# Performance work log

Measured on AMD Instinct MI355X. Metric: run time of the kernel, lower is better.

## Reference

```python
import jax, jax.numpy as jnp
import numpy as np
import math

N_HEADS = 16
D_EFF = 64
ROPE_BASE = 500.0


def _rope(x, cos, sin):
    # x: (b, h, L, d_eff); cos/sin: (L, d_eff//2)
    x_even = x[..., 0::2]
    x_odd = x[..., 1::2]
    rot = jnp.stack([x_even * cos - x_odd * sin,
                     x_even * sin + x_odd * cos], axis=-1)
    return rot.reshape(x.shape)


def setup_inputs() -> dict:
    key = jax.random.key(0)
    ks = jax.random.split(key, 5)
    B, L, D = 1, 2048, 1024
    X = jax.random.normal(ks[0], (B, L, D), dtype=jnp.float32)
    # causal mask (1 = keep, 0 = masked), broadcastable to (B, h, L, L)
    mask = jnp.tril(jnp.ones((L, L), dtype=jnp.int32))[None, :, :]
    s = 1.0 / math.sqrt(D)
    Wq = jax.random.normal(ks[1], (D, D), dtype=jnp.float32) * s
    Wk = jax.random.normal(ks[2], (D, D), dtype=jnp.float32) * s
    Wv = jax.random.normal(ks[3], (D, D), dtype=jnp.float32) * s
    Wo = jax.random.normal(ks[4], (D, D), dtype=jnp.float32) * s
    return {"X": X, "mask": mask, "Wq": Wq, "Wk": Wk, "Wv": Wv, "Wo": Wo}


def reference(X, mask, Wq, Wk, Wv, Wo):
    b, L, d_model = X.shape
    h, d = N_HEADS, D_EFF
    d_full = h * d

    def split_heads(Y):
        return Y.reshape(b, L, h, d).transpose(0, 2, 1, 3)  # (b,h,L,d)

    Q = split_heads(X @ Wq)
    K = split_heads(X @ Wk)
    V = split_heads(X @ Wv)

    # interleaved RoPE, base 500
    inv_freq = 1.0 / (ROPE_BASE ** (jnp.arange(0, d, 2, dtype=jnp.float32) / d))
    freqs = jnp.arange(L, dtype=jnp.float32)[:, None] * inv_freq  # (L, d/2)
    cos, sin = jnp.cos(freqs), jnp.sin(freqs)
    Q = _rope(Q, cos, sin)
    K = _rope(K, cos, sin)

    S = jnp.einsum('bhqd,bhkd->bhqk', Q, K) / math.sqrt(d)
    S = jnp.where(mask[:, None, :, :] == 0, jnp.float32(-1e9), S)
    # NOTE: faithful to original torch code: softmax over the HEADS axis (dim=1)
    A = jax.nn.softmax(S, axis=1)
    Y = jnp.einsum('bhqk,bhkd->bhqd', A, V)
    Y = Y.transpose(0, 2, 1, 3).reshape(b, L, d_full)
    Y = Y @ Wo
    return Y * math.sqrt(d_model / d_full)
```

## Files before the change

### kernel.cpp

```cpp
#include <hip/hip_runtime.h>
#include <stdint.h>
#include <stddef.h>

typedef __attribute__((ext_vector_type(8))) short bf16x8;
typedef __attribute__((ext_vector_type(4))) short short4v;
typedef __attribute__((ext_vector_type(4))) float f32x4;

__device__ __forceinline__ short f2bf(float f) {
  union { float f; uint32_t u; } x; x.f = f;
  return (short)((x.u + 0x7fffu + ((x.u >> 16) & 1u)) >> 16);
}
__device__ __forceinline__ float bf2f(short s) {
  union { uint32_t u; float f; } x; x.u = ((uint32_t)(uint16_t)s) << 16;
  return x.f;
}

__device__ __forceinline__ void gload_lds16(const void* g, void* lds) {
  __builtin_amdgcn_global_load_lds(
      (const __attribute__((address_space(1))) void*)g,
      (__attribute__((address_space(3))) void*)lds, 16, 0, 0);
}

__global__ __launch_bounds__(256) void cast_b(const float* __restrict__ s,
                                              short* __restrict__ d) {
  int i4 = (blockIdx.x * 256 + threadIdx.x) * 4;
  float4 v = *(const float4*)&s[i4];
  short4v r = { f2bf(v.x), f2bf(v.y), f2bf(v.z), f2bf(v.w) };
  *(short4v*)&d[i4] = r;
}

__global__ __launch_bounds__(256) void cast_add4(const short* __restrict__ Y0,
                                                 const short* __restrict__ Y1,
                                                 const short* __restrict__ Y2,
                                                 const short* __restrict__ Y3,
                                                 const float* __restrict__ Cvs,
                                                 short* __restrict__ o) {
  int i4 = (blockIdx.x * 256 + threadIdx.x) * 4;
  short4v a = *(const short4v*)&Y0[i4];
  short4v b = *(const short4v*)&Y1[i4];
  short4v c = *(const short4v*)&Y2[i4];
  short4v d = *(const short4v*)&Y3[i4];
  short4v r;
#pragma unroll
  for (int j = 0; j < 4; j++) {
    float s = bf2f(a[j]) + bf2f(b[j]) + bf2f(c[j]) + bf2f(d[j]) +
              Cvs[(i4 + j) & 1023];
    r[j] = f2bf(s);
  }
  *(short4v*)&o[i4] = r;
}

__global__ __launch_bounds__(256) void transW(const float* __restrict__ Wq,
                                              const float* __restrict__ Wk,
                                              const float* __restrict__ Wv,
                                              const float* __restrict__ Wo,
                                              short* __restrict__ WcatT,
                                              short* __restrict__ WoT) {
  int z = blockIdx.z;
  const float* src = (z == 0) ? Wq : (z == 1) ? Wk : (z == 2) ? Wv : Wo;
  short* dst = (z == 3) ? WoT : WcatT + (size_t)z * 1024 * 1024;
  __shared__ float tl[32][33];
  int tx = threadIdx.x & 31, ty = threadIdx.x >> 5;
  int kk0 = blockIdx.x * 32;
  int nn0 = blockIdx.y * 32;
#pragma unroll
  for (int j = 0; j < 4; j++)
    tl[ty + j * 8][tx] = src[(size_t)(kk0 + ty + j * 8) * 1024 + nn0 + tx];
  __syncthreads();
#pragma unroll
  for (int j = 0; j < 4; j++)
    dst[(size_t)(nn0 + ty + j * 8) * 1024 + kk0 + tx] = f2bf(tl[tx][ty + j * 8]);
}

__global__ __launch_bounds__(256) void transpose_v(const short* __restrict__ Vb,
                                                   short* __restrict__ Vt) {
  __shared__ short tv[64][72];
  int h = blockIdx.y, k0 = blockIdx.x * 64;
  int tid = threadIdx.x;
#pragma unroll
  for (int j = 0; j < 2; j++) {
    int idx = tid + j * 256;
    int row = idx >> 3, c = idx & 7;
    bf16x8 v = *(const bf16x8*)&Vb[((size_t)h * 2048 + k0 + row) * 64 + c * 8];
#pragma unroll
    for (int t = 0; t < 8; t++) tv[row][c * 8 + t] = v[t];
  }
  __syncthreads();
#pragma unroll
  for (int j = 0; j < 2; j++) {
    int idx = tid + j * 256;
    int d = idx >> 3, c = idx & 7;
    bf16x8 v;
#pragma unroll
    for (int t = 0; t < 8; t++) v[t] = tv[c * 8 + t][d];
    *(bf16x8*)&Vt[((size_t)h * 64 + d) * 2048 + k0 + c * 8] = v;
  }
}

__global__ __launch_bounds__(256) void vsum(const short* __restrict__ Vb,
                                            float* __restrict__ Cvs) {
  __shared__ float red[16][17];
  int h = blockIdx.x >> 2, dq = blockIdx.x & 3;
  int dl = threadIdx.x & 15, ks = threadIdx.x >> 4;
  int d = dq * 16 + dl;
  float acc = 0.f;
  const short* base = &Vb[((size_t)h * 2048 + ks * 128) * 64 + d];
#pragma unroll 8
  for (int k = 0; k < 128; k++) acc += bf2f(base[(size_t)k * 64]);
  red[dl][ks] = acc;
  __syncthreads();
  if (threadIdx.x < 16) {
    float sum = 0.f;
#pragma unroll
    for (int i = 0; i < 16; i++) sum += red[threadIdx.x][i];
    Cvs[h * 64 + dq * 16 + threadIdx.x] = sum * 0.0625f;
  }
}

template <int MODE, int TM>
__global__ __launch_bounds__(256, TM == 128 ? 2 : 4)
void gemm_kernel(const short* __restrict__ A, const short* __restrict__ B,
                 int N, int K, float* __restrict__ C,
                 short* __restrict__ Qb, short* __restrict__ Kb,
                 short* __restrict__ Vb) {
  constexpr int MT = TM / 32;
  constexpr int MSUB = TM / 2;
  __shared__ __attribute__((aligned(16))) short lga[TM * 64];
  __shared__ __attribute__((aligned(16))) short lgb[128 * 64];
  const int tid = threadIdx.x;
  const int lane = tid & 63;
  const int w = tid >> 6;
  const int l15 = lane & 15;
  const int quad = lane >> 4;
  const int wm = w >> 1, wn = w & 1;
  const int m0 = blockIdx.x * TM, n0 = blockIdx.y * 128;
  const int rsub = lane >> 3;
  const int cpos = lane & 7;

  f32x4 acc[MT][4];
#pragma unroll
  for (int i = 0; i < MT; i++)
#pragma unroll
    for (int j = 0; j < 4; j++) acc[i][j] = (f32x4){0.f, 0.f, 0.f, 0.f};

  for (int kb = 0; kb < K; kb += 64) {
    __syncthreads();
#pragma unroll
    for (int j = 0; j < TM / 32; j++) {
      int ci = w * (TM / 32) + j;
      int r = ci * 8 + rsub;
      int kc = cpos ^ rsub;
      gload_lds16(A + (size_t)(m0 + r) * K + kb + kc * 8, &lga[ci * 512]);
    }
#pragma unroll
    for (int j = 0; j < 4; j++) {
      int ci = w * 4 + j;
      int r = ci * 8 + rsub;
      int kc = cpos ^ rsub;
      gload_lds16(B + (size_t)(n0 + r) * K + kb + kc * 8, &lgb[ci * 512]);
    }
    __syncthreads();
#pragma unroll
    for (int kk = 0; kk < 2; kk++) {
      bf16x8 af[MT], bfr[4];
#pragma unroll
      for (int t = 0; t < MT; t++) {
        int row = wm * MSUB + t * 16 + l15;
        int pc = (kk * 4 + quad) ^ (row & 7);
        af[t] = *(const bf16x8*)&lga[row * 64 + pc * 8];
      }
#pragma unroll
      for (int t = 0; t < 4; t++) {
        int rowb = wn * 64 + t * 16 + l15;
        int pcb = (kk * 4 + quad) ^ (rowb & 7);
        bfr[t] = *(const bf16x8*)&lgb[rowb * 64 + pcb * 8];
      }
#pragma unroll
      for (int mt = 0; mt < MT; mt++)
#pragma unroll
        for (int nt = 0; nt < 4; nt++)
          acc[mt][nt] = __builtin_amdgcn_mfma_f32_16x16x32_bf16(
              af[mt], bfr[nt], acc[mt][nt], 0, 0, 0);
    }
  }

  if (MODE == 0) {
#pragma unroll
    for (int mt = 0; mt < MT; mt++) {
      int q = m0 + wm * MSUB + mt * 16 + quad * 4;
#pragma unroll
      for (int nt = 0; nt < 4; nt++) {
        int n = n0 + wn * 64 + nt * 16 + l15;
#pragma unroll
        for (int r = 0; r < 4; r++) C[(size_t)(q + r) * N + n] = acc[mt][nt][r];
      }
    }
  } else {
#pragma unroll
    for (int mt = 0; mt < MT; mt++) {
#pragma unroll
      for (int nt = 0; nt < 4; nt++) {
        int n = n0 + wn * 64 + nt * 16 + l15;
        int mat = n >> 10;
        int h = (n >> 6) & 15;
        int d = n & 63;
#pragma unroll
        for (int r = 0; r < 4; r++) {
          int q = m0 + wm * MSUB + mt * 16 + quad * 4 + r;
          float v = acc[mt][nt][r];
          float o = __shfl_xor(v, 1, 64);
          if (mat < 2) {
            int i = d >> 1;
            float ang = (float)q * __builtin_exp2f(-(float)i * 0.2801807588956902f);
            float sn, cs;
            __sincosf(ang, &sn, &cs);
            float rv = (d & 1) ? (o * sn + v * cs) : (v * cs - o * sn);
            short* dst = (mat == 0) ? Qb : Kb;
            dst[((size_t)h * 2048 + q) * 64 + d] = f2bf(rv);
          } else {
            Vb[((size_t)h * 2048 + q) * 64 + d] = f2bf(v);
          }
        }
      }
    }
  }
}

__global__ __launch_bounds__(1024, 8)
void attn_kernel(const short* __restrict__ Qb, const short* __restrict__ Kb,
                 const short* __restrict__ Vt, short* __restrict__ Yp) {
  __shared__ short Sb[16 * 16 * 72];
  const int tid = threadIdx.x;
  const int lane = tid & 63;
  const int h = tid >> 6;
  const int l15 = lane & 15, quad = lane >> 4;
  const int bx = blockIdx.x;
  const int qt = 127 - (bx >> 2);
  const int s = bx & 3;
  const int q0 = qt * 16;
  const int G = (qt + 4) >> 2;

  bf16x8 qf[2];
#pragma unroll
  for (int c = 0; c < 2; c++)
    qf[c] = *(const bf16x8*)&Qb[((size_t)h * 2048 + q0 + l15) * 64 + c * 32 + quad * 8];

  f32x4 yacc[4];
#pragma unroll
  for (int j = 0; j < 4; j++) yacc[j] = (f32x4){0.f, 0.f, 0.f, 0.f};

  const int sq = tid >> 6;
  const int sbase = sq * 72 + lane;

  for (int g = s; g < G; g += 4) {
    const int k0 = g * 64;
#pragma unroll
    for (int st = 0; st < 4; st++) {
      const short* kb = &Kb[((size_t)h * 2048 + k0 + st * 16 + l15) * 64 + quad * 8];
      bf16x8 kf0 = *(const bf16x8*)kb;
      bf16x8 kf1 = *(const bf16x8*)(kb + 32);
      f32x4 sa = (f32x4){0.f, 0.f, 0.f, 0.f};
      sa = __builtin_amdgcn_mfma_f32_16x16x32_bf16(qf[0], kf0, sa, 0, 0, 0);
      sa = __builtin_amdgcn_mfma_f32_16x16x32_bf16(qf[1], kf1, sa, 0, 0, 0);
#pragma unroll
      for (int r = 0; r < 4; r++)
        Sb[h * 1152 + (quad * 4 + r) * 72 + st * 16 + l15] =
            f2bf(sa[r] * 0.1803368801f);
    }
    __syncthreads();
    {
      bool msk = (k0 + lane) > (q0 + sq);
      float e[16];
      float sum = 0.f;
#pragma unroll
      for (int hh = 0; hh < 16; hh++) {
        e[hh] = __builtin_exp2f(bf2f(Sb[hh * 1152 + sbase]));
        sum += e[hh];
      }
      float rs = 1.f / sum;
#pragma unroll
      for (int hh = 0; hh < 16; hh++)
        Sb[hh * 1152 + sbase] = msk ? (short)0 : f2bf(e[hh] * rs - 0.0625f);
    }
    __syncthreads();
#pragma unroll
    for (int kk = 0; kk < 2; kk++) {
      bf16x8 af = *(const bf16x8*)&Sb[(h * 16 + l15) * 72 + kk * 32 + quad * 8];
#pragma unroll
      for (int nt = 0; nt < 4; nt++) {
        bf16x8 vf = *(const bf16x8*)&Vt[((size_t)h * 64 + nt * 16 + l15) * 2048 +
                                        k0 + kk * 32 + quad * 8];
        yacc[nt] = __builtin_amdgcn_mfma_f32_16x16x32_bf16(af, vf, yacc[nt], 0, 0, 0);
      }
    }
    __syncthreads();
  }
  short* Y = Yp + (size_t)s * 2048 * 1024;
#pragma unroll
  for (int nt = 0; nt < 4; nt++) {
    int col = h * 64 + nt * 16 + l15;
#pragma unroll
    for (int r = 0; r < 4; r++)
      Y[(size_t)(q0 + quad * 4 + r) * 1024 + col] = f2bf(yacc[nt][r]);
  }
}

extern "C" void kernel_launch(void* const* d_in, const int* in_sizes, int n_in,
                              void* d_out, int out_size, void* d_ws, size_t ws_size,
                              hipStream_t stream) {
  (void)in_sizes; (void)n_in; (void)out_size; (void)ws_size;
  const float* X  = (const float*)d_in[0];
  const float* Wq = (const float*)d_in[2];
  const float* Wk = (const float*)d_in[3];
  const float* Wv = (const float*)d_in[4];
  const float* Wo = (const float*)d_in[5];
  char* ws = (char*)d_ws;
  const size_t MB = 1024 * 1024;
  short* Xbf   = (short*)(ws + 0);
  short* WcatT = (short*)(ws + 4 * MB);
  short* WoT   = (short*)(ws + 10 * MB);
  short* Qb    = (short*)(ws + 12 * MB);
  short* Kb    = (short*)(ws + 16 * MB);
  short* Vb    = (short*)(ws + 20 * MB);
  short* Vt    = (short*)(ws + 24 * MB);
  short* Yp    = (short*)(ws + 28 * MB);
  float* Cvs   = (float*)(ws + 44 * MB);
  short* Ycbf  = Xbf;
  float* out   = (float*)d_out;

  cast_b<<<dim3(2048), dim3(256), 0, stream>>>(X, Xbf);
  transW<<<dim3(32, 32, 4), dim3(256), 0, stream>>>(Wq, Wk, Wv, Wo, WcatT, WoT);
  gemm_kernel<1, 128><<<dim3(16, 24), dim3(256), 0, stream>>>(
      Xbf, WcatT, 3072, 1024, nullptr, Qb, Kb, Vb);
  transpose_v<<<dim3(32, 16), dim3(256), 0, stream>>>(Vb, Vt);
  vsum<<<dim3(64), dim3(256), 0, stream>>>(Vb, Cvs);
  attn_kernel<<<dim3(512), dim3(1024), 0, stream>>>(Qb, Kb, Vt, Yp);
  cast_add4<<<dim3(2048), dim3(256), 0, stream>>>(Yp, Yp + 2048 * 1024,
                                                  Yp + 2 * 2048 * 1024,
                                                  Yp + 3 * 2048 * 1024, Cvs, Ycbf);
  gemm_kernel<0, 64><<<dim3(32, 8), dim3(256), 0, stream>>>(
      Ycbf, WoT, 1024, 1024, out, nullptr, nullptr, nullptr);
}
```

Before: 235.6 us.

## Enlarge attention query tile to 64 and reduce key splits via float atomics

The attention kernel now processes 64 query rows per block (four 16-row tiles) against 32-key chunks, so each K and V fragment load is reused across four MFMA row tiles. The key range is split eight ways across blocks, and partial outputs are combined with float atomicAdd into a zeroed fp32 buffer instead of four bf16 partial buffers. This lets the final combine kernel read one fp32 array. The cost is an extra memset, atomic contention and nondeterministic summation order, plus more registers per thread with a lower occupancy hint.

Result: slower. 256.5 us (+8.9%).

```diff
diff --git a/kernel.cpp b/kernel.cpp
--- a/kernel.cpp
+++ b/kernel.cpp
@@ -29,24 +29,15 @@
   *(short4v*)&d[i4] = r;
 }
 
-__global__ __launch_bounds__(256) void cast_add4(const short* __restrict__ Y0,
-                                                 const short* __restrict__ Y1,
-                                                 const short* __restrict__ Y2,
-                                                 const short* __restrict__ Y3,
+__global__ __launch_bounds__(256) void cast_addY(const float* __restrict__ Y,
                                                  const float* __restrict__ Cvs,
                                                  short* __restrict__ o) {
   int i4 = (blockIdx.x * 256 + threadIdx.x) * 4;
-  short4v a = *(const short4v*)&Y0[i4];
-  short4v b = *(const short4v*)&Y1[i4];
-  short4v c = *(const short4v*)&Y2[i4];
-  short4v d = *(const short4v*)&Y3[i4];
-  short4v r;
-#pragma unroll
-  for (int j = 0; j < 4; j++) {
-    float s = bf2f(a[j]) + bf2f(b[j]) + bf2f(c[j]) + bf2f(d[j]) +
-              Cvs[(i4 + j) & 1023];
-    r[j] = f2bf(s);
-  }
+  float4 v = *(const float4*)&Y[i4];
+  short4v r = { f2bf(v.x + Cvs[i4 & 1023]),
+                f2bf(v.y + Cvs[(i4 + 1) & 1023]),
+                f2bf(v.z + Cvs[(i4 + 2) & 1023]),
+                f2bf(v.w + Cvs[(i4 + 3) & 1023]) };
   *(short4v*)&o[i4] = r;
 }
 
@@ -226,82 +217,97 @@
   }
 }
 
-__global__ __launch_bounds__(1024, 8)
+__global__ __launch_bounds__(1024, 4)
 void attn_kernel(const short* __restrict__ Qb, const short* __restrict__ Kb,
-                 const short* __restrict__ Vt, short* __restrict__ Yp) {
-  __shared__ short Sb[16 * 16 * 72];
+                 const short* __restrict__ Vt, float* __restrict__ Y) {
+  __shared__ short Sb[16 * 64 * 40];
   const int tid = threadIdx.x;
   const int lane = tid & 63;
   const int h = tid >> 6;
   const int l15 = lane & 15, quad = lane >> 4;
-  const int bx = blockIdx.x;
-  const int qt = 127 - (bx >> 2);
-  const int s = bx & 3;
-  const int q0 = qt * 16;
-  const int G = (qt + 4) >> 2;
-
-  bf16x8 qf[2];
-#pragma unroll
-  for (int c = 0; c < 2; c++)
-    qf[c] = *(const bf16x8*)&Qb[((size_t)h * 2048 + q0 + l15) * 64 + c * 32 + quad * 8];
-
-  f32x4 yacc[4];
-#pragma unroll
-  for (int j = 0; j < 4; j++) yacc[j] = (f32x4){0.f, 0.f, 0.f, 0.f};
-
-  const int sq = tid >> 6;
-  const int sbase = sq * 72 + lane;
-
-  for (int g = s; g < G; g += 4) {
-    const int k0 = g * 64;
-#pragma unroll
-    for (int st = 0; st < 4; st++) {
+  const int qt = 31 - (blockIdx.x >> 3);
+  const int s = blockIdx.x & 7;
+  const int q0 = qt * 64;
+  const int C = 2 * qt + 2;
+
+  bf16x8 qf[4][2];
+#pragma unroll
+  for (int mt = 0; mt < 4; mt++)
+#pragma unroll
+    for (int c = 0; c < 2; c++)
+      qf[mt][c] = *(const bf16x8*)&Qb[((size_t)h * 2048 + q0 + mt * 16 + l15) * 64 +
+                                      c * 32 + quad * 8];
+
+  f32x4 yacc[4][4];
+#pragma unroll
+  for (int i = 0; i < 4; i++)
+#pragma unroll
+    for (int j = 0; j < 4; j++) yacc[i][j] = (f32x4){0.f, 0.f, 0.f, 0.f};
+
+  for (int g = s; g < C; g += 8) {
+    const int k0 = g * 32;
+#pragma unroll
+    for (int st = 0; st < 2; st++) {
       const short* kb = &Kb[((size_t)h * 2048 + k0 + st * 16 + l15) * 64 + quad * 8];
       bf16x8 kf0 = *(const bf16x8*)kb;
       bf16x8 kf1 = *(const bf16x8*)(kb + 32);
-      f32x4 sa = (f32x4){0.f, 0.f, 0.f, 0.f};
-      sa = __builtin_amdgcn_mfma_f32_16x16x32_bf16(qf[0], kf0, sa, 0, 0, 0);
-      sa = __builtin_amdgcn_mfma_f32_16x16x32_bf16(qf[1], kf1, sa, 0, 0, 0);
-#pragma unroll
-      for (int r = 0; r < 4; r++)
-        Sb[h * 1152 + (quad * 4 + r) * 72 + st * 16 + l15] =
-            f2bf(sa[r] * 0.1803368801f);
-    }
-    __syncthreads();
-    {
-      bool msk = (k0 + lane) > (q0 + sq);
+#pragma unroll
+      for (int mt = 0; mt < 4; mt++) {
+        f32x4 sa = (f32x4){0.f, 0.f, 0.f, 0.f};
+        sa = __builtin_amdgcn_mfma_f32_16x16x32_bf16(qf[mt][0], kf0, sa, 0, 0, 0);
+        sa = __builtin_amdgcn_mfma_f32_16x16x32_bf16(qf[mt][1], kf1, sa, 0, 0, 0);
+#pragma unroll
+        for (int r = 0; r < 4; r++)
+          Sb[(h * 64 + mt * 16 + quad * 4 + r) * 40 + st * 16 + l15] =
+              f2bf(sa[r] * 0.1803368801f);
+      }
+    }
+    __syncthreads();
+#pragma unroll
+    for (int pp = 0; pp < 2; pp++) {
+      int p = tid + pp * 1024;
+      int q = p >> 5, kl = p & 31;
+      int base = q * 40 + kl;
       float e[16];
       float sum = 0.f;
 #pragma unroll
       for (int hh = 0; hh < 16; hh++) {
-        e[hh] = __builtin_exp2f(bf2f(Sb[hh * 1152 + sbase]));
+        e[hh] = __builtin_exp2f(bf2f(Sb[hh * 2560 + base]));
         sum += e[hh];
       }
       float rs = 1.f / sum;
+      bool msk = (k0 + kl) > (q0 + q);
 #pragma unroll
       for (int hh = 0; hh < 16; hh++)
-        Sb[hh * 1152 + sbase] = msk ? (short)0 : f2bf(e[hh] * rs - 0.0625f);
-    }
-    __syncthreads();
-#pragma unroll
-    for (int kk = 0; kk < 2; kk++) {
-      bf16x8 af = *(const bf16x8*)&Sb[(h * 16 + l15) * 72 + kk * 32 + quad * 8];
+        Sb[hh * 2560 + base] = msk ? (short)0 : f2bf(e[hh] * rs - 0.0625f);
+    }
+    __syncthreads();
+    bf16x8 vf[4];
+#pragma unroll
+    for (int nt = 0; nt < 4; nt++)
+      vf[nt] = *(const bf16x8*)&Vt[((size_t)(h * 64 + nt * 16 + l15)) * 2048 +
+                                   k0 + quad * 8];
+#pragma unroll
+    for (int mt = 0; mt < 4; mt++) {
+      bf16x8 af = *(const bf16x8*)&Sb[(h * 64 + mt * 16 + l15) * 40 + quad * 8];
+#pragma unroll
+      for (int nt = 0; nt < 4; nt++)
+        yacc[mt][nt] = __builtin_amdgcn_mfma_f32_16x16x32_bf16(af, vf[nt],
+                                                               yacc[mt][nt], 0, 0, 0);
+    }
+    __syncthreads();
+  }
+  if (s < C) {
+#pragma unroll
+    for (int mt = 0; mt < 4; mt++)
 #pragma unroll
       for (int nt = 0; nt < 4; nt++) {
-        bf16x8 vf = *(const bf16x8*)&Vt[((size_t)h * 64 + nt * 16 + l15) * 2048 +
-                                        k0 + kk * 32 + quad * 8];
-        yacc[nt] = __builtin_amdgcn_mfma_f32_16x16x32_bf16(af, vf, yacc[nt], 0, 0, 0);
-      }
-    }
-    __syncthreads();
-  }
-  short* Y = Yp + (size_t)s * 2048 * 1024;
-#pragma unroll
-  for (int nt = 0; nt < 4; nt++) {
-    int col = h * 64 + nt * 16 + l15;
-#pragma unroll
-    for (int r = 0; r < 4; r++)
-      Y[(size_t)(q0 + quad * 4 + r) * 1024 + col] = f2bf(yacc[nt][r]);
+        int col = h * 64 + nt * 16 + l15;
+#pragma unroll
+        for (int r = 0; r < 4; r++)
+          atomicAdd(&Y[(size_t)(q0 + mt * 16 + quad * 4 + r) * 1024 + col],
+                    yacc[mt][nt][r]);
+      }
   }
 }
 
@@ -323,21 +329,20 @@
   short* Kb    = (short*)(ws + 16 * MB);
   short* Vb    = (short*)(ws + 20 * MB);
   short* Vt    = (short*)(ws + 24 * MB);
-  short* Yp    = (short*)(ws + 28 * MB);
-  float* Cvs   = (float*)(ws + 44 * MB);
+  float* Y     = (float*)(ws + 28 * MB);
+  float* Cvs   = (float*)(ws + 36 * MB);
   short* Ycbf  = Xbf;
   float* out   = (float*)d_out;
 
+  hipMemsetAsync(Y, 0, 8 * MB, stream);
   cast_b<<<dim3(2048), dim3(256), 0, stream>>>(X, Xbf);
   transW<<<dim3(32, 32, 4), dim3(256), 0, stream>>>(Wq, Wk, Wv, Wo, WcatT, WoT);
   gemm_kernel<1, 128><<<dim3(16, 24), dim3(256), 0, stream>>>(
       Xbf, WcatT, 3072, 1024, nullptr, Qb, Kb, Vb);
   transpose_v<<<dim3(32, 16), dim3(256), 0, stream>>>(Vb, Vt);
   vsum<<<dim3(64), dim3(256), 0, stream>>>(Vb, Cvs);
-  attn_kernel<<<dim3(512), dim3(1024), 0, stream>>>(Qb, Kb, Vt, Yp);
-  cast_add4<<<dim3(2048), dim3(256), 0, stream>>>(Yp, Yp + 2048 * 1024,
-                                                  Yp + 2 * 2048 * 1024,
-                                                  Yp + 3 * 2048 * 1024, Cvs, Ycbf);
+  attn_kernel<<<dim3(256), dim3(1024), 0, stream>>>(Qb, Kb, Vt, Y);
+  cast_addY<<<dim3(2048), dim3(256), 0, stream>>>(Y, Cvs, Ycbf);
   gemm_kernel<0, 64><<<dim3(32, 8), dim3(256), 0, stream>>>(
       Ycbf, WoT, 1024, 1024, out, nullptr, nullptr, nullptr);
 }
```

## Write V transposed from QKV GEMM, fold scale into Q, vectorize softmax LDS

Applied to the files above, without the earlier changes.

The QKV GEMM epilogue now writes V directly in transposed layout with packed 4-element stores, so the separate transpose_v kernel and the strided vsum are replaced by a simple row-reduction kernel over Vt. The attention score scale is folded into Q at projection time. In attention, the QK MFMA operands are swapped so each lane stores packed 4-wide score rows, and the cross-head softmax is done by half the threads, each handling two adjacent keys with 32-bit LDS accesses. This removes one launch and extra memory passes, at the cost of recomputing exp2 in the softmax and leaving half of the threads idle during that phase.

Result: slower. 258.4 us (+9.7%).

```diff
diff --git a/kernel.cpp b/kernel.cpp
--- a/kernel.cpp
+++ b/kernel.cpp
@@ -72,49 +72,21 @@
     dst[(size_t)(nn0 + ty + j * 8) * 1024 + kk0 + tx] = f2bf(tl[tx][ty + j * 8]);
 }
 
-__global__ __launch_bounds__(256) void transpose_v(const short* __restrict__ Vb,
-                                                   short* __restrict__ Vt) {
-  __shared__ short tv[64][72];
-  int h = blockIdx.y, k0 = blockIdx.x * 64;
-  int tid = threadIdx.x;
-#pragma unroll
-  for (int j = 0; j < 2; j++) {
-    int idx = tid + j * 256;
-    int row = idx >> 3, c = idx & 7;
-    bf16x8 v = *(const bf16x8*)&Vb[((size_t)h * 2048 + k0 + row) * 64 + c * 8];
-#pragma unroll
-    for (int t = 0; t < 8; t++) tv[row][c * 8 + t] = v[t];
-  }
-  __syncthreads();
-#pragma unroll
-  for (int j = 0; j < 2; j++) {
-    int idx = tid + j * 256;
-    int d = idx >> 3, c = idx & 7;
-    bf16x8 v;
-#pragma unroll
-    for (int t = 0; t < 8; t++) v[t] = tv[c * 8 + t][d];
-    *(bf16x8*)&Vt[((size_t)h * 64 + d) * 2048 + k0 + c * 8] = v;
-  }
-}
-
-__global__ __launch_bounds__(256) void vsum(const short* __restrict__ Vb,
+__global__ __launch_bounds__(64) void vsumT(const short* __restrict__ Vt,
                                             float* __restrict__ Cvs) {
-  __shared__ float red[16][17];
-  int h = blockIdx.x >> 2, dq = blockIdx.x & 3;
-  int dl = threadIdx.x & 15, ks = threadIdx.x >> 4;
-  int d = dq * 16 + dl;
+  int row = blockIdx.x;
+  int t = threadIdx.x;
+  const short* p = &Vt[(size_t)row * 2048];
   float acc = 0.f;
-  const short* base = &Vb[((size_t)h * 2048 + ks * 128) * 64 + d];
-#pragma unroll 8
-  for (int k = 0; k < 128; k++) acc += bf2f(base[(size_t)k * 64]);
-  red[dl][ks] = acc;
-  __syncthreads();
-  if (threadIdx.x < 16) {
-    float sum = 0.f;
-#pragma unroll
-    for (int i = 0; i < 16; i++) sum += red[threadIdx.x][i];
-    Cvs[h * 64 + dq * 16 + threadIdx.x] = sum * 0.0625f;
-  }
+#pragma unroll
+  for (int j = 0; j < 4; j++) {
+    bf16x8 v = *(const bf16x8*)&p[(t + j * 64) * 8];
+#pragma unroll
+    for (int i = 0; i < 8; i++) acc += bf2f(v[i]);
+  }
+#pragma unroll
+  for (int off = 32; off; off >>= 1) acc += __shfl_down(acc, off, 64);
+  if (t == 0) Cvs[row] = acc * 0.0625f;
 }
 
 template <int MODE, int TM>
@@ -122,7 +94,7 @@
 void gemm_kernel(const short* __restrict__ A, const short* __restrict__ B,
                  int N, int K, float* __restrict__ C,
                  short* __restrict__ Qb, short* __restrict__ Kb,
-                 short* __restrict__ Vb) {
+                 short* __restrict__ Vt) {
   constexpr int MT = TM / 32;
   constexpr int MSUB = TM / 2;
   __shared__ __attribute__((aligned(16))) short lga[TM * 64];
@@ -204,9 +176,11 @@
         int mat = n >> 10;
         int h = (n >> 6) & 15;
         int d = n & 63;
+        int qr = m0 + wm * MSUB + mt * 16 + quad * 4;
+        short4v vpk;
 #pragma unroll
         for (int r = 0; r < 4; r++) {
-          int q = m0 + wm * MSUB + mt * 16 + quad * 4 + r;
+          int q = qr + r;
           float v = acc[mt][nt][r];
           float o = __shfl_xor(v, 1, 64);
           if (mat < 2) {
@@ -215,12 +189,15 @@
             float sn, cs;
             __sincosf(ang, &sn, &cs);
             float rv = (d & 1) ? (o * sn + v * cs) : (v * cs - o * sn);
+            if (mat == 0) rv *= 0.1803368801f;
             short* dst = (mat == 0) ? Qb : Kb;
             dst[((size_t)h * 2048 + q) * 64 + d] = f2bf(rv);
           } else {
-            Vb[((size_t)h * 2048 + q) * 64 + d] = f2bf(v);
+            vpk[r] = f2bf(v);
           }
         }
+        if (mat == 2)
+          *(short4v*)&Vt[((size_t)(h * 64 + d)) * 2048 + qr] = vpk;
       }
     }
   }
@@ -234,9 +211,8 @@
   const int lane = tid & 63;
   const int h = tid >> 6;
   const int l15 = lane & 15, quad = lane >> 4;
-  const int bx = blockIdx.x;
-  const int qt = 127 - (bx >> 2);
-  const int s = bx & 3;
+  const int qt = 127 - (blockIdx.x >> 2);
+  const int s = blockIdx.x & 3;
   const int q0 = qt * 16;
   const int G = (qt + 4) >> 2;
 
@@ -249,38 +225,54 @@
 #pragma unroll
   for (int j = 0; j < 4; j++) yacc[j] = (f32x4){0.f, 0.f, 0.f, 0.f};
 
-  const int sq = tid >> 6;
-  const int sbase = sq * 72 + lane;
+  const bool sm = tid < 512;
+  const int sq = (tid >> 5) & 15;
+  const int sk2 = (tid & 31) * 2;
+  const int sbase = sq * 72 + sk2;
+
+  const short* kb0 = &Kb[(size_t)h * 2048 * 64];
+  const short* vb0 = &Vt[(size_t)h * 64 * 2048];
 
   for (int g = s; g < G; g += 4) {
     const int k0 = g * 64;
 #pragma unroll
     for (int st = 0; st < 4; st++) {
-      const short* kb = &Kb[((size_t)h * 2048 + k0 + st * 16 + l15) * 64 + quad * 8];
+      const short* kb = &kb0[(size_t)(k0 + st * 16 + l15) * 64 + quad * 8];
       bf16x8 kf0 = *(const bf16x8*)kb;
       bf16x8 kf1 = *(const bf16x8*)(kb + 32);
       f32x4 sa = (f32x4){0.f, 0.f, 0.f, 0.f};
-      sa = __builtin_amdgcn_mfma_f32_16x16x32_bf16(qf[0], kf0, sa, 0, 0, 0);
-      sa = __builtin_amdgcn_mfma_f32_16x16x32_bf16(qf[1], kf1, sa, 0, 0, 0);
-#pragma unroll
-      for (int r = 0; r < 4; r++)
-        Sb[h * 1152 + (quad * 4 + r) * 72 + st * 16 + l15] =
-            f2bf(sa[r] * 0.1803368801f);
-    }
-    __syncthreads();
-    {
-      bool msk = (k0 + lane) > (q0 + sq);
-      float e[16];
-      float sum = 0.f;
+      sa = __builtin_amdgcn_mfma_f32_16x16x32_bf16(kf0, qf[0], sa, 0, 0, 0);
+      sa = __builtin_amdgcn_mfma_f32_16x16x32_bf16(kf1, qf[1], sa, 0, 0, 0);
+      short4v pk = { f2bf(sa[0]), f2bf(sa[1]), f2bf(sa[2]), f2bf(sa[3]) };
+      *(short4v*)&Sb[(h * 16 + l15) * 72 + st * 16 + quad * 4] = pk;
+    }
+    __syncthreads();
+    if (sm) {
+      uint32_t raw[16];
+      float sum0 = 0.f, sum1 = 0.f;
 #pragma unroll
       for (int hh = 0; hh < 16; hh++) {
-        e[hh] = __builtin_exp2f(bf2f(Sb[hh * 1152 + sbase]));
-        sum += e[hh];
-      }
-      float rs = 1.f / sum;
-#pragma unroll
-      for (int hh = 0; hh < 16; hh++)
-        Sb[hh * 1152 + sbase] = msk ? (short)0 : f2bf(e[hh] * rs - 0.0625f);
+        uint32_t v = *(const uint32_t*)&Sb[hh * 1152 + sbase];
+        raw[hh] = v;
+        union { uint32_t u; float f; } lo, hi;
+        lo.u = v << 16; hi.u = v & 0xffff0000u;
+        sum0 += __builtin_exp2f(lo.f);
+        sum1 += __builtin_exp2f(hi.f);
+      }
+      float rs0 = 1.f / sum0, rs1 = 1.f / sum1;
+      bool mk0 = (k0 + sk2) > (q0 + sq);
+      bool mk1 = (k0 + sk2 + 1) > (q0 + sq);
+#pragma unroll
+      for (int hh = 0; hh < 16; hh++) {
+        uint32_t v = raw[hh];
+        union { uint32_t u; float f; } lo, hi;
+        lo.u = v << 16; hi.u = v & 0xffff0000u;
+        float a0 = __builtin_exp2f(lo.f) * rs0 - 0.0625f;
+        float a1 = __builtin_exp2f(hi.f) * rs1 - 0.0625f;
+        uint32_t w0 = mk0 ? 0u : (uint32_t)(uint16_t)f2bf(a0);
+        uint32_t w1 = mk1 ? 0u : (uint32_t)(uint16_t)f2bf(a1);
+        *(uint32_t*)&Sb[hh * 1152 + sbase] = w0 | (w1 << 16);
+      }
     }
     __syncthreads();
 #pragma unroll
@@ -288,8 +280,8 @@
       bf16x8 af = *(const bf16x8*)&Sb[(h * 16 + l15) * 72 + kk * 32 + quad * 8];
 #pragma unroll
       for (int nt = 0; nt < 4; nt++) {
-        bf16x8 vf = *(const bf16x8*)&Vt[((size_t)h * 64 + nt * 16 + l15) * 2048 +
-                                        k0 + kk * 32 + quad * 8];
+        bf16x8 vf = *(const bf16x8*)&vb0[(size_t)(nt * 16 + l15) * 2048 +
+                                         k0 + kk * 32 + quad * 8];
         yacc[nt] = __builtin_amdgcn_mfma_f32_16x16x32_bf16(af, vf, yacc[nt], 0, 0, 0);
       }
     }
@@ -321,19 +313,17 @@
   short* WoT   = (short*)(ws + 10 * MB);
   short* Qb    = (short*)(ws + 12 * MB);
   short* Kb    = (short*)(ws + 16 * MB);
-  short* Vb    = (short*)(ws + 20 * MB);
-  short* Vt    = (short*)(ws + 24 * MB);
-  short* Yp    = (short*)(ws + 28 * MB);
-  float* Cvs   = (float*)(ws + 44 * MB);
+  short* Vt    = (short*)(ws + 20 * MB);
+  short* Yp    = (short*)(ws + 24 * MB);
+  float* Cvs   = (float*)(ws + 40 * MB);
   short* Ycbf  = Xbf;
   float* out   = (float*)d_out;
 
   cast_b<<<dim3(2048), dim3(256), 0, stream>>>(X, Xbf);
   transW<<<dim3(32, 32, 4), dim3(256), 0, stream>>>(Wq, Wk, Wv, Wo, WcatT, WoT);
   gemm_kernel<1, 128><<<dim3(16, 24), dim3(256), 0, stream>>>(
-      Xbf, WcatT, 3072, 1024, nullptr, Qb, Kb, Vb);
-  transpose_v<<<dim3(32, 16), dim3(256), 0, stream>>>(Vb, Vt);
-  vsum<<<dim3(64), dim3(256), 0, stream>>>(Vb, Cvs);
+      Xbf, WcatT, 3072, 1024, nullptr, Qb, Kb, Vt);
+  vsumT<<<dim3(1024), dim3(64), 0, stream>>>(Vt, Cvs);
   attn_kernel<<<dim3(512), dim3(1024), 0, stream>>>(Qb, Kb, Vt, Yp);
   cast_add4<<<dim3(2048), dim3(256), 0, stream>>>(Yp, Yp + 2048 * 1024,
                                                   Yp + 2 * 2048 * 1024,
```
